# Kernel tuning notes

Measured on AMD Instinct MI355X. Metric: run time of the kernel, lower is better.

## Reference

```python
import jax, jax.numpy as jnp
import numpy as np

B, S, D, V = 2, 2048, 1024, 32000
EPS_LN = 1e-5
EPS_BN = 1e-5


def setup_inputs() -> dict:
    key = jax.random.key(0)
    ks = jax.random.split(key, 8)
    s = lambda k, shape: jax.random.normal(k, shape, jnp.float32) * 0.02
    return dict(
        X=jax.random.randint(ks[0], (B, S), 0, V, dtype=jnp.int32),
        emb=s(ks[1], (V, D)),
        w_hg=s(ks[2], (D, 2 * D)),            # minGRU to_hidden_and_gate (bias-free)
        conv_w=s(ks[3], (D, D, 3)),           # Conv1d OIW
        conv_b=jnp.zeros((D,), jnp.float32),
        bn_g=jnp.ones((D,), jnp.float32), bn_b=jnp.zeros((D,), jnp.float32),
        ln_g=jnp.ones((D,), jnp.float32), ln_b=jnp.zeros((D,), jnp.float32),
        w1=s(ks[4], (D, 2 * D)), b1=jnp.zeros((2 * D,), jnp.float32),
        w2=s(ks[5], (2 * D, 2 * D)), b2=jnp.zeros((2 * D,), jnp.float32),
        w3=s(ks[6], (2 * D, V)), b3=jnp.zeros((V,), jnp.float32),
    )


def _log_g(x):
    # log of g(x) = where(x>=0, x+0.5, sigmoid(x))
    return jnp.where(x >= 0, jnp.log(jax.nn.relu(x) + 0.5), -jax.nn.softplus(-x))


def _min_gru(x, w_hg):
    # Heinsen log-space associative scan (lucidrains minGRU, expansion=1)
    hg = x @ w_hg                              # [B,S,2D]
    hidden, gate = jnp.split(hg, 2, axis=-1)
    log_coeffs = -jax.nn.softplus(gate)        # log(1 - z)
    log_values = -jax.nn.softplus(-gate) + _log_g(hidden)  # log z + log h~
    a_star = jnp.cumsum(log_coeffs, axis=1)
    log_h = a_star + jax.lax.cumlogsumexp(log_values - a_star, axis=1)
    return jnp.exp(log_h)                      # [B,S,D]


def reference(X, emb, w_hg, conv_w, conv_b, bn_g, bn_b, ln_g, ln_b,
              w1, b1, w2, b2, w3, b3):
    x = emb[X]                                 # [B,S,D]
    shortcut = x
    h = _min_gru(x, w_hg)                      # dropout rate 0 -> identity
    mu = jnp.mean(h, axis=-1, keepdims=True)
    var = jnp.mean((h - mu) ** 2, axis=-1, keepdims=True)
    h = (h - mu) / jnp.sqrt(var + EPS_LN) * ln_g + ln_b
    x = h + shortcut
    xc = jnp.transpose(x, (0, 2, 1))           # [B,D,S]
    xc = jax.lax.conv_general_dilated(
        xc, conv_w, window_strides=(1,), padding=[(1, 1)],
        dimension_numbers=('NCW', 'OIW', 'NCW')) + conv_b[None, :, None]
    m = jnp.mean(xc, axis=(0, 2), keepdims=True)       # BN training-mode stats
    v = jnp.mean((xc - m) ** 2, axis=(0, 2), keepdims=True)
    xc = (xc - m) / jnp.sqrt(v + EPS_BN) * bn_g[None, :, None] + bn_b[None, :, None]
    x = jnp.transpose(xc, (0, 2, 1))           # [B,S,D]
    x = jax.nn.relu(x @ w1 + b1)
    x = jax.nn.relu(x @ w2 + b2)
    return x @ w3 + b3                         # [B,S,V]
```

## Files before the change

### kernel.cpp

```cpp
#include <hip/hip_runtime.h>
#include <hip/hip_bf16.h>

#define B_  2
#define S_  2048
#define D_  1024
#define V_  32000
#define BS_ 4096

typedef __attribute__((ext_vector_type(4))) float f32x4;
typedef __attribute__((ext_vector_type(8))) short short8;
typedef unsigned long long u64;
typedef unsigned short u16;

__device__ __forceinline__ u16 f2bf(float x) {
  unsigned int u = __float_as_uint(x);
  u += 0x7FFFu + ((u >> 16) & 1u);
  return (u16)(u >> 16);
}
__device__ __forceinline__ u64 pack4bf(float a, float b, float c, float d) {
  return (u64)f2bf(a) | ((u64)f2bf(b) << 16) | ((u64)f2bf(c) << 32) | ((u64)f2bf(d) << 48);
}

#define GLOAD_LDS16(g, l) __builtin_amdgcn_global_load_lds( \
    (const __attribute__((address_space(1))) void*)(g),     \
    (__attribute__((address_space(3))) void*)(l), 16, 0, 0)

template<bool RELU, bool BF16OUT, bool HASBIAS>
__global__ __launch_bounds__(256) void gemm_bt(
    const u16* __restrict__ A, const u16* __restrict__ Bt,
    const float* __restrict__ bias, void* __restrict__ Cout,
    int M, int N, int K)
{
  __shared__ __attribute__((aligned(16))) u16 Alds[128 * 64];
  __shared__ __attribute__((aligned(16))) u16 Blds[128 * 64];
  const int tid = threadIdx.x;
  const int w = tid >> 6, l = tid & 63;
  const int wr = w >> 1, wc = w & 1;
  const int m0 = blockIdx.y * 128, n0 = blockIdx.x * 128;
  const int lr = l >> 3, lc = l & 7;
  const int fr = l & 15, fq = l >> 4;

  const u16* Ag = A + (size_t)(m0 + w * 8 + lr) * K + lc * 8;
  const u16* Bg = Bt + (size_t)(n0 + w * 8 + lr) * K + lc * 8;

  f32x4 acc[4][4];
#pragma unroll
  for (int i = 0; i < 4; ++i)
#pragma unroll
    for (int j = 0; j < 4; ++j) acc[i][j] = {0.f, 0.f, 0.f, 0.f};

  for (int kt = 0; kt < K; kt += 64) {
#pragma unroll
    for (int r = 0; r < 4; ++r) {
      GLOAD_LDS16(Ag + (size_t)(r * 32) * K + kt, &Alds[(r * 32 + w * 8) * 64]);
      GLOAD_LDS16(Bg + (size_t)(r * 32) * K + kt, &Blds[(r * 32 + w * 8) * 64]);
    }
    __syncthreads();
#pragma unroll
    for (int ks = 0; ks < 2; ++ks) {
      short8 af[4], bfv[4];
#pragma unroll
      for (int i = 0; i < 4; ++i)
        af[i] = *reinterpret_cast<const short8*>(
            &Alds[(wr * 64 + i * 16 + fr) * 64 + ks * 32 + fq * 8]);
#pragma unroll
      for (int j = 0; j < 4; ++j)
        bfv[j] = *reinterpret_cast<const short8*>(
            &Blds[(wc * 64 + j * 16 + fr) * 64 + ks * 32 + fq * 8]);
#pragma unroll
      for (int i = 0; i < 4; ++i)
#pragma unroll
        for (int j = 0; j < 4; ++j)
          acc[i][j] = __builtin_amdgcn_mfma_f32_16x16x32_bf16(af[i], bfv[j], acc[i][j], 0, 0, 0);
    }
    __syncthreads();
  }

  const int row0 = m0 + wr * 64 + fq * 4;
  const int col0 = n0 + wc * 64 + fr;
#pragma unroll
  for (int j = 0; j < 4; ++j) {
    const int col = col0 + j * 16;
    const float bv = HASBIAS ? bias[col] : 0.f;
#pragma unroll
    for (int i = 0; i < 4; ++i) {
#pragma unroll
      for (int r = 0; r < 4; ++r) {
        const int row = row0 + i * 16 + r;
        float v = acc[i][j][r] + bv;
        if (RELU) v = fmaxf(v, 0.f);
        if (BF16OUT) ((u16*)Cout)[(size_t)row * N + col] = f2bf(v);
        else         ((float*)Cout)[(size_t)row * N + col] = v;
      }
    }
  }
}

#define AOFF(b, h) (((b) * 4 + (h)) * 8192)
#define BOFF(b, h) (((b) * 4 + 2 + (h)) * 8192)
#define FENCE() asm volatile("" ::: "memory")
#define BARRIER() do { FENCE(); __builtin_amdgcn_s_barrier(); FENCE(); } while (0)
#define WAIT_LGKM0() asm volatile("s_waitcnt lgkmcnt(0)" ::: "memory")

template<bool RELU, bool BF16OUT, bool HASBIAS>
__global__ __launch_bounds__(512, 2) void gemm256_bt(
    const u16* __restrict__ A, const u16* __restrict__ Bt,
    const float* __restrict__ bias, void* __restrict__ Cout,
    int M, int N, int K, int CW)
{
  __shared__ __attribute__((aligned(16))) u16 LDS[65536];
  const int tid = threadIdx.x;
  const int w = tid >> 6, l = tid & 63;
  const int wr = w >> 2, wc = w & 3;
  const int fr = l & 15, fq = l >> 4;

  const int MTt = M >> 8;
  const int bpc = MTt * CW;
  const int chunk = blockIdx.x / bpc, rem = blockIdx.x % bpc;
  const int m0 = (rem % MTt) << 8;
  const int n0 = ((chunk * CW) + rem / MTt) << 8;

  const int NT = K >> 6;
  const u16* Abase = A + (size_t)m0 * K;
  const u16* Bbase = Bt + (size_t)n0 * K;

  const int rq_[2] = { w * 16 + (l >> 3), w * 16 + 8 + (l >> 3) };
  const int gq_[2] = { (l & 7) ^ (rq_[0] & 7), (l & 7) ^ (rq_[1] & 7) };

#define STAGE_HALF(matbase, h, t, ldsoff) do {                               \
  _Pragma("unroll")                                                          \
  for (int q_ = 0; q_ < 2; ++q_)                                             \
    GLOAD_LDS16((matbase) + ((size_t)((h) * 128 + rq_[q_])) * K +            \
                    (size_t)(t) * 64 + gq_[q_] * 8,                          \
                &LDS[(ldsoff) + (w * 128 + q_ * 64) * 8]);                   \
} while (0)

#define READ_A(arr, bufb, q_) do {                                           \
  _Pragma("unroll")                                                          \
  for (int i_ = 0; i_ < 4; ++i_) {                                           \
    const int r_ = (q_) * 64 + i_ * 16 + fr;                                 \
    _Pragma("unroll")                                                        \
    for (int ks_ = 0; ks_ < 2; ++ks_)                                        \
      arr[i_][ks_] = *reinterpret_cast<const short8*>(                       \
          &LDS[AOFF(bufb, wr) + r_ * 64 + ((ks_ * 4 + fq) ^ (fr & 7)) * 8]); \
  } } while (0)

#define READ_B(arr, bufb, jq_) do {                                          \
  _Pragma("unroll")                                                          \
  for (int j_ = 0; j_ < 2; ++j_) {                                           \
    const int r_ = (wc & 1) * 64 + (jq_) * 32 + j_ * 16 + fr;                \
    _Pragma("unroll")                                                        \
    for (int ks_ = 0; ks_ < 2; ++ks_)                                        \
      arr[j_][ks_] = *reinterpret_cast<const short8*>(                       \
          &LDS[BOFF(bufb, wc >> 1) + r_ * 64 +                               \
               ((ks_ * 4 + fq) ^ (fr & 7)) * 8]);                            \
  } } while (0)

#define MFMA_Q(arrA, arrB, itb, jtb) do {                                    \
  _Pragma("unroll")                                                          \
  for (int i_ = 0; i_ < 4; ++i_)                                             \
    _Pragma("unroll")                                                        \
    for (int j_ = 0; j_ < 2; ++j_)                                           \
      _Pragma("unroll")                                                      \
      for (int ks_ = 0; ks_ < 2; ++ks_)                                      \
        acc[(itb) + i_][(jtb) + j_] = __builtin_amdgcn_mfma_f32_16x16x32_bf16( \
            arrA[i_][ks_], arrB[j_][ks_], acc[(itb) + i_][(jtb) + j_], 0, 0, 0); \
} while (0)

  f32x4 acc[8][4];
#pragma unroll
  for (int i = 0; i < 8; ++i)
#pragma unroll
    for (int j = 0; j < 4; ++j) acc[i][j] = {0.f, 0.f, 0.f, 0.f};

  STAGE_HALF(Abase, 0, 0, AOFF(0, 0));
  STAGE_HALF(Abase, 1, 0, AOFF(0, 1));
  STAGE_HALF(Bbase, 0, 0, BOFF(0, 0));
  STAGE_HALF(Bbase, 1, 0, BOFF(0, 1));
  if (NT > 1) {
    STAGE_HALF(Bbase, 0, 1, BOFF(1, 0));
    STAGE_HALF(Abase, 0, 1, AOFF(1, 0));
    asm volatile("s_waitcnt vmcnt(4)" ::: "memory");
  } else {
    asm volatile("s_waitcnt vmcnt(0)" ::: "memory");
  }
  BARRIER();

  for (int t = 0; t < NT; ++t) {
    const int cb = t & 1, nb = cb ^ 1;
    short8 a0[4][2], a1[4][2], b0[2][2], b1[2][2];

    READ_A(a0, cb, 0);
    READ_B(b0, cb, 0);
    if (t + 1 < NT) STAGE_HALF(Abase, 1, t + 1, AOFF(nb, 1));
    BARRIER(); WAIT_LGKM0();
    __builtin_amdgcn_s_setprio(1);
    MFMA_Q(a0, b0, 0, 0);
    __builtin_amdgcn_s_setprio(0);
    BARRIER();

    READ_B(b1, cb, 1);
    if (t + 1 < NT) STAGE_HALF(Bbase, 1, t + 1, BOFF(nb, 1));
    BARRIER(); WAIT_LGKM0();
    __builtin_amdgcn_s_setprio(1);
    MFMA_Q(a0, b1, 0, 2);
    __builtin_amdgcn_s_setprio(0);
    BARRIER();

    READ_A(a1, cb, 1);
    if (t + 2 < NT) STAGE_HALF(Bbase, 0, t + 2, BOFF(cb, 0));
    BARRIER(); WAIT_LGKM0();
    __builtin_amdgcn_s_setprio(1);
    MFMA_Q(a1, b1, 4, 2);
    __builtin_amdgcn_s_setprio(0);
    BARRIER();

    if (t + 2 < NT) STAGE_HALF(Abase, 0, t + 2, AOFF(cb, 0));
    BARRIER(); WAIT_LGKM0();
    __builtin_amdgcn_s_setprio(1);
    MFMA_Q(a1, b0, 4, 0);
    __builtin_amdgcn_s_setprio(0);
    if (t + 2 < NT) { asm volatile("s_waitcnt vmcnt(4)" ::: "memory"); }
    else            { asm volatile("s_waitcnt vmcnt(0)" ::: "memory"); }
    BARRIER();
  }

  const int row0 = m0 + wr * 128 + fq * 4;
  const int col0 = n0 + wc * 64 + fr;
#pragma unroll
  for (int jt = 0; jt < 4; ++jt) {
    const int col = col0 + jt * 16;
    const float bv = HASBIAS ? bias[col] : 0.f;
#pragma unroll
    for (int it = 0; it < 8; ++it) {
#pragma unroll
      for (int rr = 0; rr < 4; ++rr) {
        const int row = row0 + it * 16 + rr;
        float v = acc[it][jt][rr] + bv;
        if (RELU) v = fmaxf(v, 0.f);
        if (BF16OUT) ((u16*)Cout)[(size_t)row * N + col] = f2bf(v);
        else         ((float*)Cout)[(size_t)row * N + col] = v;
      }
    }
  }
#undef STAGE_HALF
#undef READ_A
#undef READ_B
#undef MFMA_Q
}

__global__ __launch_bounds__(256) void transpose_f2b(
    const float* __restrict__ in, u16* __restrict__ out, int K, int N)
{
  __shared__ float t[32][33];
  const int n0 = blockIdx.x * 32, k0 = blockIdx.y * 32;
  const int r = threadIdx.x >> 5, cc = threadIdx.x & 31;
#pragma unroll
  for (int rr = 0; rr < 4; ++rr) {
    const int ki = rr * 8 + r;
    t[ki][cc] = in[(size_t)(k0 + ki) * N + n0 + cc];
  }
  __syncthreads();
#pragma unroll
  for (int rr = 0; rr < 4; ++rr) {
    const int ni = rr * 8 + r;
    out[(size_t)(n0 + ni) * K + k0 + cc] = f2bf(t[cc][ni]);
  }
}

__global__ __launch_bounds__(256) void convw_reorder(
    const float* __restrict__ cw, u16* __restrict__ out)
{
  const int gid = blockIdx.x * 256 + threadIdx.x;
  const int o = gid >> 10, i = gid & 1023;
  const float w0 = cw[(size_t)gid * 3 + 0];
  const float w1 = cw[(size_t)gid * 3 + 1];
  const float w2 = cw[(size_t)gid * 3 + 2];
  out[(size_t)o * 3072 + i]          = f2bf(w0);
  out[(size_t)o * 3072 + 1024 + i]   = f2bf(w1);
  out[(size_t)o * 3072 + 2048 + i]   = f2bf(w2);
}

__global__ __launch_bounds__(256) void gather_emb(
    const int* __restrict__ X, const float* __restrict__ emb, u16* __restrict__ xb)
{
  const int row = blockIdx.x;
  const int tok = X[row];
  const int d4 = threadIdx.x * 4;
  const float4 v = *reinterpret_cast<const float4*>(emb + (size_t)tok * D_ + d4);
  *(u64*)(&xb[(size_t)row * D_ + d4]) = pack4bf(v.x, v.y, v.z, v.w);
}

#define GRU_CP(hid_, gate_, h_, cp_) {                                   \
  const float t_ = __expf(-(gate_));                                     \
  const float z_ = 1.f / (1.f + t_);                                     \
  const float c_ = t_ * z_;                                              \
  const float g_ = ((hid_) >= 0.f) ? ((hid_) + 0.5f)                     \
                                   : (1.f / (1.f + __expf(-(hid_))));    \
  (h_) = c_ * (h_) + z_ * g_; (cp_) *= c_; }

#define GRU_NC(hid_, gate_, h_) {                                        \
  const float t_ = __expf(-(gate_));                                     \
  const float z_ = 1.f / (1.f + t_);                                     \
  const float g_ = ((hid_) >= 0.f) ? ((hid_) + 0.5f)                     \
                                   : (1.f / (1.f + __expf(-(hid_))));    \
  (h_) = (t_ * z_) * (h_) + z_ * g_; }

__global__ __launch_bounds__(256) void scan_partial(
    const float* __restrict__ hg, float* __restrict__ Cb, float* __restrict__ Vb)
{
  const int b = blockIdx.x >> 6, c = blockIdx.x & 63;
  const int d4 = threadIdx.x * 4;
  const float* base = hg + ((size_t)b * S_ + (size_t)c * 32) * (2 * D_);
  float h[4] = {0.f, 0.f, 0.f, 0.f}, cp[4] = {1.f, 1.f, 1.f, 1.f};
  for (int t = 0; t < 32; ++t) {
    const float4 hd = *reinterpret_cast<const float4*>(base + (size_t)t * (2 * D_) + d4);
    const float4 gt = *reinterpret_cast<const float4*>(base + (size_t)t * (2 * D_) + D_ + d4);
    GRU_CP(hd.x, gt.x, h[0], cp[0]); GRU_CP(hd.y, gt.y, h[1], cp[1]);
    GRU_CP(hd.z, gt.z, h[2], cp[2]); GRU_CP(hd.w, gt.w, h[3], cp[3]);
  }
  const size_t o = ((size_t)(b * 64 + c)) * D_ + d4;
  *(float4*)(Cb + o) = make_float4(cp[0], cp[1], cp[2], cp[3]);
  *(float4*)(Vb + o) = make_float4(h[0], h[1], h[2], h[3]);
}

__global__ void scan_carry(const float* __restrict__ Cb, const float* __restrict__ Vb,
                           float* __restrict__ Hs)
{
  const int gid = blockIdx.x * 256 + threadIdx.x;
  const int b = gid >> 10, d = gid & 1023;
  float h = 0.f;
  for (int c = 0; c < 64; ++c) {
    const size_t o = ((size_t)(b * 64 + c)) * D_ + d;
    Hs[o] = h;
    h = Cb[o] * h + Vb[o];
  }
}

__global__ __launch_bounds__(256) void scan_emit(
    const float* __restrict__ hg, const float* __restrict__ Hs,
    const int* __restrict__ X, const float* __restrict__ emb,
    const float* __restrict__ ln_g, const float* __restrict__ ln_b,
    u16* __restrict__ Aconv)
{
  __shared__ float red[4];
  const int b = blockIdx.x >> 6, c = blockIdx.x & 63;
  const int tid = threadIdx.x;
  const int w = tid >> 6, l = tid & 63;
  const int d4 = tid * 4;
  const float* base = hg + ((size_t)b * S_ + (size_t)c * 32) * (2 * D_);
  float h0, h1, h2, h3;
  {
    const float4 hs = *reinterpret_cast<const float4*>(Hs + ((size_t)(b * 64 + c)) * D_ + d4);
    h0 = hs.x; h1 = hs.y; h2 = hs.z; h3 = hs.w;
  }
  const float4 lg = *reinterpret_cast<const float4*>(ln_g + d4);
  const float4 lb = *reinterpret_cast<const float4*>(ln_b + d4);

  for (int t = 0; t < 32; ++t) {
    const int s = c * 32 + t;
    const float4 hd = *reinterpret_cast<const float4*>(base + (size_t)t * (2 * D_) + d4);
    const float4 gt = *reinterpret_cast<const float4*>(base + (size_t)t * (2 * D_) + D_ + d4);
    GRU_NC(hd.x, gt.x, h0); GRU_NC(hd.y, gt.y, h1);
    GRU_NC(hd.z, gt.z, h2); GRU_NC(hd.w, gt.w, h3);

    float sm = h0 + h1 + h2 + h3;
#pragma unroll
    for (int m = 1; m < 64; m <<= 1) sm += __shfl_xor(sm, m);
    __syncthreads();
    if (l == 0) red[w] = sm;
    __syncthreads();
    const float mu = (red[0] + red[1] + red[2] + red[3]) * (1.f / (float)D_);
    float q = (h0 - mu) * (h0 - mu) + (h1 - mu) * (h1 - mu) +
              (h2 - mu) * (h2 - mu) + (h3 - mu) * (h3 - mu);
#pragma unroll
    for (int m = 1; m < 64; m <<= 1) q += __shfl_xor(q, m);
    __syncthreads();
    if (l == 0) red[w] = q;
    __syncthreads();
    const float var = (red[0] + red[1] + red[2] + red[3]) * (1.f / (float)D_);
    const float rstd = rsqrtf(var + 1e-5f);

    const int tok = X[b * S_ + s];
    const float4 e = *reinterpret_cast<const float4*>(emb + (size_t)tok * D_ + d4);
    const float x0 = (h0 - mu) * rstd * lg.x + lb.x + e.x;
    const float x1 = (h1 - mu) * rstd * lg.y + lb.y + e.y;
    const float x2 = (h2 - mu) * rstd * lg.z + lb.z + e.z;
    const float x3 = (h3 - mu) * rstd * lg.w + lb.w + e.w;
    const u64 pk = pack4bf(x0, x1, x2, x3);

    const size_t row = (size_t)b * S_ + s;
    *(u64*)(&Aconv[row * 3072 + D_ + d4]) = pk;
    if (s + 1 < S_) *(u64*)(&Aconv[(row + 1) * 3072 + d4]) = pk;
    if (s > 0)      *(u64*)(&Aconv[(row - 1) * 3072 + 2 * D_ + d4]) = pk;
    if (s == 0)       *(u64*)(&Aconv[row * 3072 + d4]) = 0ull;
    if (s == S_ - 1)  *(u64*)(&Aconv[row * 3072 + 2 * D_ + d4]) = 0ull;
  }
}

__global__ __launch_bounds__(256) void bn_partial(
    const float* __restrict__ cv, float* __restrict__ ps, float* __restrict__ pq)
{
  const int blk = blockIdx.x;
  const int c4 = threadIdx.x * 4;
  float s0 = 0, s1 = 0, s2 = 0, s3 = 0, q0 = 0, q1 = 0, q2 = 0, q3 = 0;
  for (int r = 0; r < 64; ++r) {
    const float4 v = *reinterpret_cast<const float4*>(cv + ((size_t)blk * 64 + r) * D_ + c4);
    s0 += v.x; s1 += v.y; s2 += v.z; s3 += v.w;
    q0 += v.x * v.x; q1 += v.y * v.y; q2 += v.z * v.z; q3 += v.w * v.w;
  }
  *(float4*)(ps + (size_t)blk * D_ + c4) = make_float4(s0, s1, s2, s3);
  *(float4*)(pq + (size_t)blk * D_ + c4) = make_float4(q0, q1, q2, q3);
}

__global__ void bn_finalize(const float* __restrict__ ps, const float* __restrict__ pq,
                            const float* __restrict__ bn_g, const float* __restrict__ bn_b,
                            float* __restrict__ scale, float* __restrict__ shift)
{
  const int c = blockIdx.x * 256 + threadIdx.x;
  float s = 0.f, q = 0.f;
  for (int blk = 0; blk < 64; ++blk) { s += ps[(size_t)blk * D_ + c]; q += pq[(size_t)blk * D_ + c]; }
  const float m = s * (1.f / (float)BS_);
  const float var = q * (1.f / (float)BS_) - m * m;
  const float rs = rsqrtf(var + 1e-5f);
  const float sc = bn_g[c] * rs;
  scale[c] = sc;
  shift[c] = bn_b[c] - m * sc;
}

__global__ __launch_bounds__(256) void bn_apply(
    const float* __restrict__ cv, const float* __restrict__ scale,
    const float* __restrict__ shift, u16* __restrict__ out)
{
  const size_t idx = ((size_t)blockIdx.x * 256 + threadIdx.x) * 4;
  const int c = (int)(idx & 1023);
  const float4 v = *reinterpret_cast<const float4*>(cv + idx);
  const float4 sc = *reinterpret_cast<const float4*>(scale + c);
  const float4 sh = *reinterpret_cast<const float4*>(shift + c);
  *(u64*)(&out[idx]) = pack4bf(v.x * sc.x + sh.x, v.y * sc.y + sh.y,
                               v.z * sc.z + sh.z, v.w * sc.w + sh.w);
}

extern "C" void kernel_launch(void* const* d_in, const int* in_sizes, int n_in,
                              void* d_out, int out_size, void* d_ws, size_t ws_size,
                              hipStream_t stream)
{
  const int*   X      = (const int*)d_in[0];
  const float* emb    = (const float*)d_in[1];
  const float* w_hg   = (const float*)d_in[2];
  const float* conv_w = (const float*)d_in[3];
  const float* bn_g   = (const float*)d_in[5];
  const float* bn_b   = (const float*)d_in[6];
  const float* ln_g   = (const float*)d_in[7];
  const float* ln_b   = (const float*)d_in[8];
  const float* w1     = (const float*)d_in[9];
  const float* b1     = (const float*)d_in[10];
  const float* w2     = (const float*)d_in[11];
  const float* b2     = (const float*)d_in[12];
  const float* w3     = (const float*)d_in[13];
  const float* b3     = (const float*)d_in[14];
  float* out = (float*)d_out;
  char* ws = (char*)d_ws;

  const size_t OFF_A4    = 0;
  const size_t BASE      = 16777216;
  const size_t OFF_W3T   = BASE;
  const size_t OFF_WHGT  = BASE;
  const size_t OFF_W1T   = BASE + 4194304;
  const size_t OFF_W2T   = OFF_W1T + 4194304;
  const size_t OFF_WCVT  = OFF_W2T + 8388608;
  const size_t OFF_XBF   = OFF_WCVT + 6291456;
  const size_t OFF_HG    = OFF_XBF + 8388608;
  const size_t OFF_CB    = OFF_HG + 33554432;
  const size_t OFF_VB    = OFF_CB + 524288;
  const size_t OFF_HS    = OFF_VB + 524288;
  const size_t OFF_ACONV = OFF_HS + 524288;
  const size_t OFF_CVO   = OFF_ACONV + 25165824;
  const size_t OFF_A2    = OFF_CVO + 16777216;
  const size_t OFF_A3    = OFF_A2 + 8388608;
  const size_t OFF_BNS   = OFF_A3 + 16777216;
  const size_t OFF_BNQ   = OFF_BNS + 262144;
  const size_t OFF_SC    = OFF_BNQ + 262144;
  const size_t OFF_SH    = OFF_SC + 4096;
  (void)in_sizes; (void)n_in; (void)out_size; (void)ws_size;

  u16*   WHGT = (u16*)(ws + OFF_WHGT);
  u16*   W1T  = (u16*)(ws + OFF_W1T);
  u16*   W2T  = (u16*)(ws + OFF_W2T);
  u16*   W3T  = (u16*)(ws + OFF_W3T);
  u16*   WCVT = (u16*)(ws + OFF_WCVT);
  u16*   XBF  = (u16*)(ws + OFF_XBF);
  float* HG   = (float*)(ws + OFF_HG);
  float* CB   = (float*)(ws + OFF_CB);
  float* VB   = (float*)(ws + OFF_VB);
  float* HS   = (float*)(ws + OFF_HS);
  u16*   ACONV= (u16*)(ws + OFF_ACONV);
  float* CVO  = (float*)(ws + OFF_CVO);
  u16*   A2   = (u16*)(ws + OFF_A2);
  u16*   A3   = (u16*)(ws + OFF_A3);
  u16*   A4   = (u16*)(ws + OFF_A4);
  float* BNS  = (float*)(ws + OFF_BNS);
  float* BNQ  = (float*)(ws + OFF_BNQ);
  float* SC   = (float*)(ws + OFF_SC);
  float* SH   = (float*)(ws + OFF_SH);

  transpose_f2b<<<dim3(2048 / 32, 1024 / 32), 256, 0, stream>>>(w_hg, WHGT, 1024, 2048);
  transpose_f2b<<<dim3(2048 / 32, 1024 / 32), 256, 0, stream>>>(w1,   W1T,  1024, 2048);
  transpose_f2b<<<dim3(2048 / 32, 2048 / 32), 256, 0, stream>>>(w2,   W2T,  2048, 2048);
  convw_reorder<<<4096, 256, 0, stream>>>(conv_w, WCVT);

  gather_emb<<<BS_, 256, 0, stream>>>(X, emb, XBF);

  gemm_bt<false, false, false><<<dim3(2048 / 128, BS_ / 128), 256, 0, stream>>>(
      XBF, WHGT, nullptr, HG, BS_, 2048, 1024);

  scan_partial<<<B_ * 64, 256, 0, stream>>>(HG, CB, VB);
  scan_carry<<<8, 256, 0, stream>>>(CB, VB, HS);
  scan_emit<<<B_ * 64, 256, 0, stream>>>(HG, HS, X, emb, ln_g, ln_b, ACONV);

  gemm_bt<false, false, false><<<dim3(1024 / 128, BS_ / 128), 256, 0, stream>>>(
      ACONV, WCVT, nullptr, CVO, BS_, 1024, 3072);

  bn_partial<<<64, 256, 0, stream>>>(CVO, BNS, BNQ);
  bn_finalize<<<4, 256, 0, stream>>>(BNS, BNQ, bn_g, bn_b, SC, SH);
  bn_apply<<<4096, 256, 0, stream>>>(CVO, SC, SH, A2);

  gemm_bt<true, true, true><<<dim3(2048 / 128, BS_ / 128), 256, 0, stream>>>(
      A2, W1T, b1, A3, BS_, 2048, 1024);
  gemm_bt<true, true, true><<<dim3(2048 / 128, BS_ / 128), 256, 0, stream>>>(
      A3, W2T, b2, A4, BS_, 2048, 2048);

  transpose_f2b<<<dim3(V_ / 32, 2048 / 32), 256, 0, stream>>>(w3, W3T, 2048, V_);
  gemm256_bt<false, false, true><<<dim3((BS_ / 256) * (V_ / 256)), 512, 0, stream>>>(
      A4, W3T, b3, out, BS_, V_, 2048, 16);
}
```

Measured before the change: 931.8 us.

## Stage GEMM epilogue through LDS for vector stores and pin LDS reads

The 256x256 GEMM epilogue now writes each 16-row slab of accumulators (plus bias) into a per-wave LDS scratch region. It reads them back row-contiguous, so output is written as 16-byte fp32 or 8-byte packed bf16 stores instead of scattered scalar stores. The LDS fragment loads become inline-asm ds_read_b128, and a sched_barrier after each lgkmcnt wait stops the compiler from moving instructions across it. The compiler memory fences around s_barrier are removed. The epilogue adds LDS round-trips and a block barrier per slab, and the weaker fencing relies on the asm ordering staying correct.

```diff
diff --git a/kernel.cpp b/kernel.cpp
--- a/kernel.cpp
+++ b/kernel.cpp
@@ -24,6 +24,15 @@
 #define GLOAD_LDS16(g, l) __builtin_amdgcn_global_load_lds( \
     (const __attribute__((address_space(1))) void*)(g),     \
     (__attribute__((address_space(3))) void*)(l), 16, 0, 0)
+
+__device__ __forceinline__ unsigned lds_addr32(const void* p) {
+  return (unsigned)(uintptr_t)(const __attribute__((address_space(3))) void*)p;
+}
+__device__ __forceinline__ short8 ds_read128(unsigned a) {
+  short8 r;
+  asm volatile("ds_read_b128 %0, %1" : "=&v"(r) : "v"(a));
+  return r;
+}
 
 template<bool RELU, bool BF16OUT, bool HASBIAS>
 __global__ __launch_bounds__(256) void gemm_bt(
@@ -98,9 +107,9 @@
 
 #define AOFF(b, h) (((b) * 4 + (h)) * 8192)
 #define BOFF(b, h) (((b) * 4 + 2 + (h)) * 8192)
-#define FENCE() asm volatile("" ::: "memory")
-#define BARRIER() do { FENCE(); __builtin_amdgcn_s_barrier(); FENCE(); } while (0)
-#define WAIT_LGKM0() asm volatile("s_waitcnt lgkmcnt(0)" ::: "memory")
+#define BARRIER() __builtin_amdgcn_s_barrier()
+#define WAITL0_PIN() do { asm volatile("s_waitcnt lgkmcnt(0)" ::: "memory"); \
+                          __builtin_amdgcn_sched_barrier(0); } while (0)
 
 template<bool RELU, bool BF16OUT, bool HASBIAS>
 __global__ __launch_bounds__(512, 2) void gemm256_bt(
@@ -113,6 +122,7 @@
   const int w = tid >> 6, l = tid & 63;
   const int wr = w >> 2, wc = w & 3;
   const int fr = l & 15, fq = l >> 4;
+  const unsigned ldsb = lds_addr32(&LDS[0]);
 
   const int MTt = M >> 8;
   const int bpc = MTt * CW;
@@ -141,8 +151,8 @@
     const int r_ = (q_) * 64 + i_ * 16 + fr;                                 \
     _Pragma("unroll")                                                        \
     for (int ks_ = 0; ks_ < 2; ++ks_)                                        \
-      arr[i_][ks_] = *reinterpret_cast<const short8*>(                       \
-          &LDS[AOFF(bufb, wr) + r_ * 64 + ((ks_ * 4 + fq) ^ (fr & 7)) * 8]); \
+      arr[i_][ks_] = ds_read128(ldsb + 2u * (unsigned)(AOFF(bufb, wr) +      \
+          r_ * 64 + ((ks_ * 4 + fq) ^ (fr & 7)) * 8));                       \
   } } while (0)
 
 #define READ_B(arr, bufb, jq_) do {                                          \
@@ -151,9 +161,8 @@
     const int r_ = (wc & 1) * 64 + (jq_) * 32 + j_ * 16 + fr;                \
     _Pragma("unroll")                                                        \
     for (int ks_ = 0; ks_ < 2; ++ks_)                                        \
-      arr[j_][ks_] = *reinterpret_cast<const short8*>(                       \
-          &LDS[BOFF(bufb, wc >> 1) + r_ * 64 +                               \
-               ((ks_ * 4 + fq) ^ (fr & 7)) * 8]);                            \
+      arr[j_][ks_] = ds_read128(ldsb + 2u * (unsigned)(BOFF(bufb, wc >> 1) + \
+          r_ * 64 + ((ks_ * 4 + fq) ^ (fr & 7)) * 8));                       \
   } } while (0)
 
 #define MFMA_Q(arrA, arrB, itb, jtb) do {                                    \
@@ -193,7 +202,7 @@
     READ_A(a0, cb, 0);
     READ_B(b0, cb, 0);
     if (t + 1 < NT) STAGE_HALF(Abase, 1, t + 1, AOFF(nb, 1));
-    BARRIER(); WAIT_LGKM0();
+    BARRIER(); WAITL0_PIN();
     __builtin_amdgcn_s_setprio(1);
     MFMA_Q(a0, b0, 0, 0);
     __builtin_amdgcn_s_setprio(0);
@@ -201,7 +210,7 @@
 
     READ_B(b1, cb, 1);
     if (t + 1 < NT) STAGE_HALF(Bbase, 1, t + 1, BOFF(nb, 1));
-    BARRIER(); WAIT_LGKM0();
+    BARRIER(); WAITL0_PIN();
     __builtin_amdgcn_s_setprio(1);
     MFMA_Q(a0, b1, 0, 2);
     __builtin_amdgcn_s_setprio(0);
@@ -209,14 +218,14 @@
 
     READ_A(a1, cb, 1);
     if (t + 2 < NT) STAGE_HALF(Bbase, 0, t + 2, BOFF(cb, 0));
-    BARRIER(); WAIT_LGKM0();
+    BARRIER(); WAITL0_PIN();
     __builtin_amdgcn_s_setprio(1);
     MFMA_Q(a1, b1, 4, 2);
     __builtin_amdgcn_s_setprio(0);
     BARRIER();
 
     if (t + 2 < NT) STAGE_HALF(Abase, 0, t + 2, AOFF(cb, 0));
-    BARRIER(); WAIT_LGKM0();
+    BARRIER(); WAITL0_PIN();
     __builtin_amdgcn_s_setprio(1);
     MFMA_Q(a1, b0, 4, 0);
     __builtin_amdgcn_s_setprio(0);
@@ -225,23 +234,37 @@
     BARRIER();
   }
 
-  const int row0 = m0 + wr * 128 + fq * 4;
-  const int col0 = n0 + wc * 64 + fr;
-#pragma unroll
-  for (int jt = 0; jt < 4; ++jt) {
-    const int col = col0 + jt * 16;
-    const float bv = HASBIAS ? bias[col] : 0.f;
-#pragma unroll
-    for (int it = 0; it < 8; ++it) {
-#pragma unroll
-      for (int rr = 0; rr < 4; ++rr) {
-        const int row = row0 + it * 16 + rr;
-        float v = acc[it][jt][rr] + bv;
-        if (RELU) v = fmaxf(v, 0.f);
-        if (BF16OUT) ((u16*)Cout)[(size_t)row * N + col] = f2bf(v);
-        else         ((float*)Cout)[(size_t)row * N + col] = v;
+  float* lf = (float*)(void*)(&LDS[0]) + (size_t)w * 1088;
+  const int row_base = m0 + wr * 128;
+  const int col_base = n0 + wc * 64;
+  float bvv[4];
+#pragma unroll
+  for (int jt = 0; jt < 4; ++jt)
+    bvv[jt] = HASBIAS ? bias[col_base + jt * 16 + fr] : 0.f;
+  const int er = l >> 4, ec = (l & 15) * 4;
+#pragma unroll
+  for (int it = 0; it < 8; ++it) {
+#pragma unroll
+    for (int jt = 0; jt < 4; ++jt)
+#pragma unroll
+      for (int rr = 0; rr < 4; ++rr)
+        lf[(fq * 4 + rr) * 68 + jt * 16 + fr] = acc[it][jt][rr] + bvv[jt];
+#pragma unroll
+    for (int ch = 0; ch < 4; ++ch) {
+      f32x4 vv = *(const f32x4*)&lf[(ch * 4 + er) * 68 + ec];
+      if (RELU) {
+        vv[0] = fmaxf(vv[0], 0.f); vv[1] = fmaxf(vv[1], 0.f);
+        vv[2] = fmaxf(vv[2], 0.f); vv[3] = fmaxf(vv[3], 0.f);
+      }
+      const int grow = row_base + it * 16 + ch * 4 + er;
+      if (BF16OUT) {
+        *(u64*)(&((u16*)Cout)[(size_t)grow * N + col_base + ec]) =
+            pack4bf(vv[0], vv[1], vv[2], vv[3]);
+      } else {
+        *(f32x4*)(&((float*)Cout)[(size_t)grow * N + col_base + ec]) = vv;
       }
     }
+    __syncthreads();
   }
 #undef STAGE_HALF
 #undef READ_A
```

Result: faster. 891.2 us (-4.4%).
